# Kernel tuning notes

Hardware: AMD Instinct MI355X
Metric: run time of the kernel (lower is better)

The kernel has to match this reference:

```python
import jax, jax.numpy as jnp
import numpy as np

TOKENS = 8192
MODEL_DIM = 4096
NUM_EXPERTS = 64
K = 2


def setup_inputs() -> dict:
    key = jax.random.key(0)
    kx, kw = jax.random.split(key)
    x = jax.random.normal(kx, (TOKENS, MODEL_DIM), dtype=jnp.float32)
    # nn.Linear default init: U(-1/sqrt(fan_in), 1/sqrt(fan_in)); weight shape [E, D]
    bound = 1.0 / np.sqrt(MODEL_DIM)
    W = jax.random.uniform(kw, (NUM_EXPERTS, MODEL_DIM), dtype=jnp.float32,
                           minval=-bound, maxval=bound)
    return {"x": x, "W": W}


def reference(x, W):
    # TopKGate.forward with k=2, eval mode (no noise): logits -> top2gating
    logits = jnp.einsum("td,ed->te", x.astype(jnp.float32), W)  # [T, E]
    # topk indices (sorted by value, like torch.topk)
    _, topi = jax.lax.top_k(logits, K)                           # [T, K]
    gates = jax.nn.softmax(logits, axis=-1)                      # [T, E]
    # (gates * one_hot(idx)).sum(-1) == gather of gates at idx
    g = jnp.take_along_axis(gates, topi, axis=-1)                # [T, K]
    eps = jnp.finfo(gates.dtype).eps
    denom = jnp.maximum(jnp.sum(g, axis=-1, keepdims=True), eps)
    g = g / denom
    # matches return ([idx1, idx2], [gate1, gate2]) with flattened indices
    return (topi[:, 0], topi[:, 1], g[:, 0], g[:, 1])
```

## Files before the change

### kernel.cpp

```cpp
#include <hip/hip_runtime.h>
#include <float.h>
#include <math.h>

#define TOKENS 8192
#define DIM    4096

typedef _Float16 v8h  __attribute__((ext_vector_type(8)));
typedef float    v4f  __attribute__((ext_vector_type(4)));

typedef __attribute__((address_space(3))) unsigned int lds_uint;
typedef const __attribute__((address_space(1))) unsigned int glob_uint;

__device__ __forceinline__ void stage16(const _Float16* g, _Float16* l) {
    __builtin_amdgcn_global_load_lds((glob_uint*)g, (lds_uint*)l, 16, 0, 0);
}

__global__ __launch_bounds__(256) void prep_w_kernel(
    const float* __restrict__ W, _Float16* __restrict__ WF) {
    int n = blockIdx.x * 256 + threadIdx.x;
    int chunk = n >> 8;
    int et    = (n >> 6) & 3;
    int lane  = n & 63;
    int e  = et * 16 + (lane & 15);
    int k0 = chunk * 32 + (lane >> 4) * 8;
    const float* src = W + (size_t)e * DIM + k0;
    v8h h, l;
    #pragma unroll
    for (int j = 0; j < 8; ++j) {
        float w = src[j];
        _Float16 wh = (_Float16)w;
        h[j] = wh;
        l[j] = (_Float16)((w - (float)wh) * 2048.0f);
    }
    size_t base = (size_t)chunk * 4096 + (size_t)et * 512 + (size_t)lane * 8;
    *(v8h*)(WF + base)        = h;
    *(v8h*)(WF + base + 2048) = l;
}

#define LOAD_A(Aa, Ab, cc) do {                                               \
    const float* ap_ = abase + (cc) * 32;                                     \
    Aa = *(const float4*)ap_;                                                 \
    Ab = *(const float4*)(ap_ + 4);                                           \
} while (0)

#define STAGE(BI, cc) stage16(sbase + (size_t)(cc) * 4096, &buf[BI][wq * 512])

#define CVT1(f, j) {                                                          \
    _Float16 h_ = (_Float16)(f);                                              \
    ah[j] = h_;                                                               \
    al[j] = (_Float16)(((f) - (float)h_) * 2048.0f);                          \
}
#define CVT(Aa, Ab) do {                                                      \
    CVT1(Aa.x, 0) CVT1(Aa.y, 1) CVT1(Aa.z, 2) CVT1(Aa.w, 3)                   \
    CVT1(Ab.x, 4) CVT1(Ab.y, 5) CVT1(Ab.z, 6) CVT1(Ab.w, 7)                   \
} while (0)

#define MFMA16(a, b, c) __builtin_amdgcn_mfma_f32_16x16x32_f16(a, b, c, 0, 0, 0)

#define COMPC(BI, Aa, Ab) do {                                                \
    CVT(Aa, Ab);                                                              \
    const _Float16* bp_ = &buf[BI][0] + (size_t)lane * 8;                     \
    v8h h0_ = *(const v8h*)(bp_);                                             \
    v8h h1_ = *(const v8h*)(bp_ + 512);                                       \
    v8h h2_ = *(const v8h*)(bp_ + 1024);                                      \
    v8h h3_ = *(const v8h*)(bp_ + 1536);                                      \
    v8h l0_ = *(const v8h*)(bp_ + 2048);                                      \
    v8h l1_ = *(const v8h*)(bp_ + 2560);                                      \
    v8h l2_ = *(const v8h*)(bp_ + 3072);                                      \
    v8h l3_ = *(const v8h*)(bp_ + 3584);                                      \
    acc1[0] = MFMA16(ah, h0_, acc1[0]);                                       \
    acc1[1] = MFMA16(ah, h1_, acc1[1]);                                       \
    acc1[2] = MFMA16(ah, h2_, acc1[2]);                                       \
    acc1[3] = MFMA16(ah, h3_, acc1[3]);                                       \
    acc2[0] = MFMA16(al, h0_, acc2[0]);  acc2[0] = MFMA16(ah, l0_, acc2[0]);  \
    acc2[1] = MFMA16(al, h1_, acc2[1]);  acc2[1] = MFMA16(ah, l1_, acc2[1]);  \
    acc2[2] = MFMA16(al, h2_, acc2[2]);  acc2[2] = MFMA16(ah, l2_, acc2[2]);  \
    acc2[3] = MFMA16(al, h3_, acc2[3]);  acc2[3] = MFMA16(ah, l3_, acc2[3]);  \
} while (0)

#define BARRIER_KEEP(n) do {                                                  \
    __builtin_amdgcn_sched_barrier(0);                                        \
    asm volatile("s_waitcnt vmcnt(" #n ")" ::: "memory");                     \
    __builtin_amdgcn_sched_barrier(0);                                        \
    __builtin_amdgcn_s_barrier();                                             \
    __builtin_amdgcn_sched_barrier(0);                                        \
} while (0)

#define ITER_FULL(c, ACa, ACb, ALa, ALb, BCUR, BNXT) do {                     \
    STAGE(BNXT, (c) + 1);                                                     \
    LOAD_A(ALa, ALb, (c) + 2);                                                \
    COMPC(BCUR, ACa, ACb);                                                    \
    BARRIER_KEEP(2);                                                          \
} while (0)

#define ITER_STAGE_ONLY(c, ACa, ACb, BCUR, BNXT) do {                         \
    STAGE(BNXT, (c) + 1);                                                     \
    COMPC(BCUR, ACa, ACb);                                                    \
    BARRIER_KEEP(0);                                                          \
} while (0)

__global__ __launch_bounds__(512, 4) void logits_kernel(
    const float* __restrict__ x,
    const _Float16* __restrict__ WF,
    float* __restrict__ P) {

    __shared__ _Float16 buf[2][4096];

    const int tid  = threadIdx.x;
    const int wq   = tid >> 6;
    const int lane = tid & 63;
    const int kg   = (int)(blockIdx.x & 7);
    const int tg   = (int)(blockIdx.x >> 3);
    const int tok0 = tg * 128 + wq * 16;
    const int art  = lane & 15;
    const int akg  = lane >> 4;
    const int chunk0 = kg * 16;

    const float*    abase = x  + (size_t)(tok0 + art) * DIM + chunk0 * 32 + akg * 8;
    const _Float16* sbase = WF + (size_t)chunk0 * 4096 + (size_t)tid * 8;

    v4f acc1[4], acc2[4];
    #pragma unroll
    for (int e4 = 0; e4 < 4; ++e4) { acc1[e4] = (v4f)0.0f; acc2[e4] = (v4f)0.0f; }

    float4 A0a, A0b, A1a, A1b, A2a, A2b;
    v8h ah, al;

    STAGE(0, 0);
    LOAD_A(A0a, A0b, 0);
    LOAD_A(A1a, A1b, 1);
    BARRIER_KEEP(4);

    ITER_FULL(0,  A0a, A0b, A2a, A2b, 0, 1);
    ITER_FULL(1,  A1a, A1b, A0a, A0b, 1, 0);
    ITER_FULL(2,  A2a, A2b, A1a, A1b, 0, 1);
    ITER_FULL(3,  A0a, A0b, A2a, A2b, 1, 0);
    ITER_FULL(4,  A1a, A1b, A0a, A0b, 0, 1);
    ITER_FULL(5,  A2a, A2b, A1a, A1b, 1, 0);
    ITER_FULL(6,  A0a, A0b, A2a, A2b, 0, 1);
    ITER_FULL(7,  A1a, A1b, A0a, A0b, 1, 0);
    ITER_FULL(8,  A2a, A2b, A1a, A1b, 0, 1);
    ITER_FULL(9,  A0a, A0b, A2a, A2b, 1, 0);
    ITER_FULL(10, A1a, A1b, A0a, A0b, 0, 1);
    ITER_FULL(11, A2a, A2b, A1a, A1b, 1, 0);
    ITER_FULL(12, A0a, A0b, A2a, A2b, 0, 1);
    ITER_FULL(13, A1a, A1b, A0a, A0b, 1, 0);
    ITER_STAGE_ONLY(14, A2a, A2b, 0, 1);
    COMPC(1, A0a, A0b);

    const float inv2048 = 1.0f / 2048.0f;
    #pragma unroll
    for (int e4 = 0; e4 < 4; ++e4) {
        #pragma unroll
        for (int r = 0; r < 4; ++r) {
            float v = acc1[e4][r] + acc2[e4][r] * inv2048;
            P[((size_t)kg * TOKENS + tok0 + akg * 4 + r) * 64 + e4 * 16 + art] = v;
        }
    }
}

__global__ __launch_bounds__(256) void reduce_topk_kernel(
    const float* __restrict__ P, float* __restrict__ out) {
    const int wq   = threadIdx.x >> 6;
    const int lane = threadIdx.x & 63;
    #pragma unroll
    for (int tt = 0; tt < 4; ++tt) {
        int gt = blockIdx.x * 16 + wq * 4 + tt;
        float v = 0.f;
        #pragma unroll
        for (int kg = 0; kg < 8; ++kg)
            v += P[((size_t)kg * TOKENS + gt) * 64 + lane];

        float bv = v; int bi = lane;
        #pragma unroll
        for (int off = 32; off >= 1; off >>= 1) {
            float ov = __shfl_xor(bv, off);
            int   oi = __shfl_xor(bi, off);
            if (ov > bv || (ov == bv && oi < bi)) { bv = ov; bi = oi; }
        }
        float v2 = (lane == bi) ? -FLT_MAX : v;
        float bv2 = v2; int bi2 = lane;
        #pragma unroll
        for (int off = 32; off >= 1; off >>= 1) {
            float ov = __shfl_xor(bv2, off);
            int   oi = __shfl_xor(bi2, off);
            if (ov > bv2 || (ov == bv2 && oi < bi2)) { bv2 = ov; bi2 = oi; }
        }

        if (lane == 0) {
            float g0 = 1.0f / (1.0f + expf(bv2 - bv));
            out[gt]              = (float)bi;
            out[TOKENS + gt]     = (float)bi2;
            out[2 * TOKENS + gt] = g0;
            out[3 * TOKENS + gt] = 1.0f - g0;
        }
    }
}

extern "C" void kernel_launch(void* const* d_in, const int* in_sizes, int n_in,
                              void* d_out, int out_size, void* d_ws, size_t ws_size,
                              hipStream_t stream) {
    const float* x = (const float*)d_in[0];
    const float* W = (const float*)d_in[1];
    float* out     = (float*)d_out;
    _Float16* WF   = (_Float16*)d_ws;
    float* P       = (float*)((char*)d_ws + (1 << 20));

    prep_w_kernel<<<128, 256, 0, stream>>>(W, WF);
    logits_kernel<<<512, 512, 0, stream>>>(x, WF, P);
    reduce_topk_kernel<<<512, 256, 0, stream>>>(P, out);
}
```

Baseline: 41.08 us.

## Fuse W fp16 split conversion into logits kernel, drop prep kernel

Removes the separate prep_w kernel that split W into fp16 hi/lo parts. The logits kernel now loads fp32 W directly with register loads, converts it in-kernel, and writes both halves into LDS each iteration, replacing the async global_load_lds staging. It also switches the x loads to nontemporal. This saves one kernel launch and the workspace round trip. In exchange, every block redoes the W conversion, and the W loads are now synchronous through registers.

```diff
diff --git a/kernel.cpp b/kernel.cpp
--- a/kernel.cpp
+++ b/kernel.cpp
@@ -6,44 +6,29 @@
 #define DIM    4096
 
 typedef _Float16 v8h  __attribute__((ext_vector_type(8)));
+typedef _Float16 v4h  __attribute__((ext_vector_type(4)));
 typedef float    v4f  __attribute__((ext_vector_type(4)));
 
-typedef __attribute__((address_space(3))) unsigned int lds_uint;
-typedef const __attribute__((address_space(1))) unsigned int glob_uint;
-
-__device__ __forceinline__ void stage16(const _Float16* g, _Float16* l) {
-    __builtin_amdgcn_global_load_lds((glob_uint*)g, (lds_uint*)l, 16, 0, 0);
-}
-
-__global__ __launch_bounds__(256) void prep_w_kernel(
-    const float* __restrict__ W, _Float16* __restrict__ WF) {
-    int n = blockIdx.x * 256 + threadIdx.x;
-    int chunk = n >> 8;
-    int et    = (n >> 6) & 3;
-    int lane  = n & 63;
-    int e  = et * 16 + (lane & 15);
-    int k0 = chunk * 32 + (lane >> 4) * 8;
-    const float* src = W + (size_t)e * DIM + k0;
-    v8h h, l;
-    #pragma unroll
-    for (int j = 0; j < 8; ++j) {
-        float w = src[j];
-        _Float16 wh = (_Float16)w;
-        h[j] = wh;
-        l[j] = (_Float16)((w - (float)wh) * 2048.0f);
-    }
-    size_t base = (size_t)chunk * 4096 + (size_t)et * 512 + (size_t)lane * 8;
-    *(v8h*)(WF + base)        = h;
-    *(v8h*)(WF + base + 2048) = l;
-}
 
 #define LOAD_A(Aa, Ab, cc) do {                                               \
     const float* ap_ = abase + (cc) * 32;                                     \
-    Aa = *(const float4*)ap_;                                                 \
-    Ab = *(const float4*)(ap_ + 4);                                           \
-} while (0)
-
-#define STAGE(BI, cc) stage16(sbase + (size_t)(cc) * 4096, &buf[BI][wq * 512])
+    Aa = __builtin_nontemporal_load((const v4f*)ap_);        \
+    Ab = __builtin_nontemporal_load((const v4f*)(ap_ + 4));                   \
+} while (0)
+
+#define LOAD_W(WV, cc) do { WV = *(const v4f*)(wsrc + (cc) * 32); } while (0)
+
+#define WRITE_W(BI, WV) do {                                                  \
+    v4h hh_, ll_;                                                             \
+    _Pragma("unroll")                                                         \
+    for (int j_ = 0; j_ < 4; ++j_) {                                          \
+        _Float16 h_ = (_Float16)WV[j_];                                       \
+        hh_[j_] = h_;                                                         \
+        ll_[j_] = (_Float16)((WV[j_] - (float)h_) * 2048.0f);                 \
+    }                                                                         \
+    *(v4h*)(&buf[BI][wofs])        = hh_;                                     \
+    *(v4h*)(&buf[BI][2048 + wofs]) = ll_;                                     \
+} while (0)
 
 #define CVT1(f, j) {                                                          \
     _Float16 h_ = (_Float16)(f);                                              \
@@ -51,8 +36,8 @@
     al[j] = (_Float16)(((f) - (float)h_) * 2048.0f);                          \
 }
 #define CVT(Aa, Ab) do {                                                      \
-    CVT1(Aa.x, 0) CVT1(Aa.y, 1) CVT1(Aa.z, 2) CVT1(Aa.w, 3)                   \
-    CVT1(Ab.x, 4) CVT1(Ab.y, 5) CVT1(Ab.z, 6) CVT1(Ab.w, 7)                   \
+    CVT1(Aa[0], 0) CVT1(Aa[1], 1) CVT1(Aa[2], 2) CVT1(Aa[3], 3)               \
+    CVT1(Ab[0], 4) CVT1(Ab[1], 5) CVT1(Ab[2], 6) CVT1(Ab[3], 7)               \
 } while (0)
 
 #define MFMA16(a, b, c) __builtin_amdgcn_mfma_f32_16x16x32_f16(a, b, c, 0, 0, 0)
@@ -78,30 +63,31 @@
     acc2[3] = MFMA16(al, h3_, acc2[3]);  acc2[3] = MFMA16(ah, l3_, acc2[3]);  \
 } while (0)
 
-#define BARRIER_KEEP(n) do {                                                  \
+#define BARRIER_LDS() do {                                                    \
+    asm volatile("s_waitcnt lgkmcnt(0)" ::: "memory");                        \
     __builtin_amdgcn_sched_barrier(0);                                        \
-    asm volatile("s_waitcnt vmcnt(" #n ")" ::: "memory");                     \
+    __builtin_amdgcn_s_barrier();                                            \
     __builtin_amdgcn_sched_barrier(0);                                        \
-    __builtin_amdgcn_s_barrier();                                             \
-    __builtin_amdgcn_sched_barrier(0);                                        \
 } while (0)
 
 #define ITER_FULL(c, ACa, ACb, ALa, ALb, BCUR, BNXT) do {                     \
-    STAGE(BNXT, (c) + 1);                                                     \
+    LOAD_W(wv, (c) + 1);                                                      \
     LOAD_A(ALa, ALb, (c) + 2);                                                \
     COMPC(BCUR, ACa, ACb);                                                    \
-    BARRIER_KEEP(2);                                                          \
-} while (0)
-
-#define ITER_STAGE_ONLY(c, ACa, ACb, BCUR, BNXT) do {                         \
-    STAGE(BNXT, (c) + 1);                                                     \
+    WRITE_W(BNXT, wv);                                                        \
+    BARRIER_LDS();                                                            \
+} while (0)
+
+#define ITER_NOA(c, ACa, ACb, BCUR, BNXT) do {           \
+    LOAD_W(wv, (c) + 1);                                                      \
     COMPC(BCUR, ACa, ACb);                                                    \
-    BARRIER_KEEP(0);                                                          \
+    WRITE_W(BNXT, wv);                                                        \
+    BARRIER_LDS();                                                            \
 } while (0)
 
 __global__ __launch_bounds__(512, 4) void logits_kernel(
     const float* __restrict__ x,
-    const _Float16* __restrict__ WF,
+    const float* __restrict__ W,
     float* __restrict__ P) {
 
     __shared__ _Float16 buf[2][4096];
@@ -116,20 +102,26 @@
     const int akg  = lane >> 4;
     const int chunk0 = kg * 16;
 
-    const float*    abase = x  + (size_t)(tok0 + art) * DIM + chunk0 * 32 + akg * 8;
-    const _Float16* sbase = WF + (size_t)chunk0 * 4096 + (size_t)tid * 8;
+    const float* abase = x + (size_t)(tok0 + art) * DIM + chunk0 * 32 + akg * 8;
+
+    const int row  = tid >> 1, half = tid & 1;
+    const int et   = row >> 6, lr = row & 63;
+    const int we   = et * 16 + (lr & 15);
+    const float* wsrc = W + (size_t)we * DIM + chunk0 * 32 + (lr >> 4) * 8 + half * 4;
+    const int wofs = et * 512 + lr * 8 + half * 4;
 
     v4f acc1[4], acc2[4];
     #pragma unroll
     for (int e4 = 0; e4 < 4; ++e4) { acc1[e4] = (v4f)0.0f; acc2[e4] = (v4f)0.0f; }
 
-    float4 A0a, A0b, A1a, A1b, A2a, A2b;
+    v4f A0a, A0b, A1a, A1b, A2a, A2b, wv;
     v8h ah, al;
 
-    STAGE(0, 0);
+    LOAD_W(wv, 0);
     LOAD_A(A0a, A0b, 0);
     LOAD_A(A1a, A1b, 1);
-    BARRIER_KEEP(4);
+    WRITE_W(0, wv);
+    BARRIER_LDS();
 
     ITER_FULL(0,  A0a, A0b, A2a, A2b, 0, 1);
     ITER_FULL(1,  A1a, A1b, A0a, A0b, 1, 0);
@@ -145,7 +137,7 @@
     ITER_FULL(11, A2a, A2b, A1a, A1b, 1, 0);
     ITER_FULL(12, A0a, A0b, A2a, A2b, 0, 1);
     ITER_FULL(13, A1a, A1b, A0a, A0b, 1, 0);
-    ITER_STAGE_ONLY(14, A2a, A2b, 0, 1);
+    ITER_NOA(14, A2a, A2b, 0, 1);
     COMPC(1, A0a, A0b);
 
     const float inv2048 = 1.0f / 2048.0f;
@@ -203,10 +195,8 @@
     const float* x = (const float*)d_in[0];
     const float* W = (const float*)d_in[1];
     float* out     = (float*)d_out;
-    _Float16* WF   = (_Float16*)d_ws;
-    float* P       = (float*)((char*)d_ws + (1 << 20));
-
-    prep_w_kernel<<<128, 256, 0, stream>>>(W, WF);
-    logits_kernel<<<512, 512, 0, stream>>>(x, WF, P);
+    float* P       = (float*)d_ws;
+
+    logits_kernel<<<512, 512, 0, stream>>>(x, W, P);
     reduce_topk_kernel<<<512, 256, 0, stream>>>(P, out);
 }
```

New measurement: 47.91 us. +16.6%, slower.
